# Performance work log

Measured on AMD Instinct MI355X. Metric: run time of the kernel, lower is better.

The kernel has to match this reference:

```python
import jax, jax.numpy as jnp
import numpy as np

EPS = 1e-5  # instance-norm epsilon (NormalizeLayer over spatial axes)

def instance_norm(x):
    # normalize over spatial axes (1,2) per sample, per channel
    mean = jnp.mean(x, axis=(1, 2), keepdims=True)
    var = jnp.var(x, axis=(1, 2), keepdims=True)
    return (x - mean) / jnp.sqrt(var + EPS)

def l2norm(x, axis=-1):
    return x / jnp.sqrt(jnp.sum(x * x, axis=axis, keepdims=True) + 1e-12)

def setup_inputs() -> dict:
    key = jax.random.key(0)
    ks = jax.random.split(key, 5)
    B, H, W, C = 4, 64, 64, 256
    content = jax.random.normal(ks[0], (B, H, W, C), jnp.float32)
    style = jax.random.normal(ks[1], (B, H, W, C), jnp.float32)
    scale = 1.0 / np.sqrt(C)
    Wq = jax.random.normal(ks[2], (C, C), jnp.float32) * scale
    Wk = jax.random.normal(ks[3], (C, C), jnp.float32) * scale
    Wv = jax.random.normal(ks[4], (C, C), jnp.float32) * scale
    bq = jnp.zeros((C,), jnp.float32)
    bk = jnp.zeros((C,), jnp.float32)
    bv = jnp.zeros((C,), jnp.float32)
    return {"content": content, "style": style, "Wq": Wq, "bq": bq,
            "Wk": Wk, "bk": bk, "Wv": Wv, "bv": bv}

def reference(content, style, Wq, bq, Wk, bk, Wv, bv):
    B, H, W, C = content.shape
    N = H * W
    norm_content = instance_norm(content)
    norm_style = instance_norm(style)
    # 1x1 convs == per-pixel linear layers
    Q = (jnp.einsum('bhwc,cd->bhwd', norm_content, Wq) + bq).reshape(B, N, C)
    K = (jnp.einsum('bhwc,cd->bhwd', norm_style, Wk) + bk).reshape(B, N, C)
    V = (jnp.einsum('bhwc,cd->bhwd', style, Wv) + bv).reshape(B, N, C)
    # cosine-similarity attention (Dot with normalize=True)
    attn = jnp.einsum('bnc,bmc->bnm', l2norm(Q), l2norm(K))  # [B, N, N]
    A = jax.nn.softmax(attn, axis=-1)
    M = jnp.einsum('bnm,bmc->bnc', A, V)                 # weighted mean
    S2 = jnp.einsum('bnm,bmc->bnc', A, V * V) - M * M    # weighted variance
    S2 = jax.nn.relu(S2)
    # safe sqrt: grad-safe at exactly 0 (matches sqrt(relu(x)) values)
    S = jnp.where(S2 > 0, jnp.sqrt(jnp.where(S2 > 0, S2, 1.0)), 0.0)
    S = S.reshape(B, H, W, C)
    M = M.reshape(B, H, W, C)
    return S * norm_content + M
```

## Files before the change

### kernel.cpp

```cpp
#include <hip/hip_runtime.h>
#include <cstdint>

#define BB 4
#define NN 4096
#define CC 256

typedef __attribute__((ext_vector_type(8))) short bf16x8;
typedef __attribute__((ext_vector_type(4))) short bf16x4;
typedef __attribute__((ext_vector_type(4))) float f32x4;
typedef unsigned int u32;
typedef __attribute__((ext_vector_type(4))) u32 u32x4;

#define MFMA_FP8(a, b, c)  __builtin_amdgcn_mfma_f32_16x16x32_fp8_fp8((a), (b), (c), 0, 0, 0)

#define WAITCNT(vm, xp, lgkm) (((vm) & 0xF) | (((vm) >> 4) << 14) | ((xp) << 4) | ((lgkm) << 8))

__device__ __forceinline__ unsigned short f2bf(float f) {
  union { float f; unsigned u; } v; v.f = f;
  unsigned r = v.u + 0x7fffu + ((v.u >> 16) & 1u);
  return (unsigned short)(r >> 16);
}
__device__ __forceinline__ u32 pk4_fp8(float a, float b, float c, float d) {
  u32 v = (u32)__builtin_amdgcn_cvt_pk_fp8_f32(a, b, 0, false);
  v = (u32)__builtin_amdgcn_cvt_pk_fp8_f32(c, d, (int)v, true);
  return v;
}
__device__ __forceinline__ unsigned char fp8_1(float a) {
  return (unsigned char)(((u32)__builtin_amdgcn_cvt_pk_fp8_f32(a, a, 0, false)) & 0xff);
}

typedef __attribute__((address_space(3))) unsigned int lds_u32;
typedef __attribute__((address_space(1))) unsigned int glb_u32;

__device__ __forceinline__ void async_cp16(const void* g, void* l) {
  __builtin_amdgcn_global_load_lds((const glb_u32*)g,
                                   (lds_u32*)(unsigned)(unsigned long long)l,
                                   16, 0, 0);
}

__global__ __launch_bounds__(256) void transpose_w(const float* __restrict__ Wq,
                                                   const float* __restrict__ Wk,
                                                   const float* __restrict__ Wv,
                                                   unsigned char* __restrict__ Wt8) {
  __shared__ float sT[64 * 65];
  int blk = blockIdx.x;
  int z = blk / 16, tl = blk % 16;
  int c0 = (tl >> 2) * 64, d0 = (tl & 3) * 64;
  const float* W = (z == 0) ? Wq : ((z == 1) ? Wk : Wv);
  #pragma unroll
  for (int i = 0; i < 16; ++i) {
    int e = i * 256 + threadIdx.x;
    int c = e >> 6, d = e & 63;
    sT[c * 65 + d] = W[(size_t)(c0 + c) * CC + d0 + d];
  }
  __syncthreads();
  #pragma unroll
  for (int i = 0; i < 16; ++i) {
    int e = i * 256 + threadIdx.x;
    int d = e >> 6, c = e & 63;
    Wt8[(size_t)z * 65536 + (size_t)(d0 + d) * CC + c0 + c] = fp8_1(sT[c * 65 + d]);
  }
}

__global__ __launch_bounds__(256) void stats_partial(const float* __restrict__ content,
                                                     const float* __restrict__ style,
                                                     float* __restrict__ sums) {
  int blk = blockIdx.x;
  int t = blk >> 9, b = (blk >> 7) & 3, chunk = blk & 127;
  const float* X = t ? style : content;
  int c = threadIdx.x;
  const float* base = X + ((size_t)b * NN + (size_t)chunk * 32) * CC + c;
  float s = 0.f, ss = 0.f;
  #pragma unroll 8
  for (int r = 0; r < 32; ++r) {
    float x = base[(size_t)r * CC];
    s += x; ss += x * x;
  }
  atomicAdd(&sums[((t * 2 + 0) * BB + b) * CC + c], s);
  atomicAdd(&sums[((t * 2 + 1) * BB + b) * CC + c], ss);
}

__global__ __launch_bounds__(256) void stats_finalize(const float* __restrict__ sums,
                                                      float* __restrict__ stats) {
  int i = blockIdx.x * 256 + threadIdx.x;
  int t = i >> 10, bc = i & 1023;
  float s = sums[(t * 2 + 0) * 1024 + bc];
  float ss = sums[(t * 2 + 1) * 1024 + bc];
  float m = s * (1.0f / NN);
  float var = ss * (1.0f / NN) - m * m;
  stats[(t * 2 + 0) * 1024 + bc] = m;
  stats[(t * 2 + 1) * 1024 + bc] = rsqrtf(var + 1e-5f);
}

__global__ __launch_bounds__(256, 2) void qkv_kernel(
    const float* __restrict__ content, const float* __restrict__ style,
    const unsigned char* __restrict__ Wt8,
    const float* __restrict__ bq, const float* __restrict__ bk, const float* __restrict__ bv,
    const float* __restrict__ stats,
    unsigned char* __restrict__ Qn, unsigned char* __restrict__ Kn,
    unsigned char* __restrict__ Vct) {
  __shared__ __align__(16) char sW[32768];
  __shared__ __align__(16) char sX[32768];

  int tid = threadIdx.x;
  int wid = tid >> 6, lane = tid & 63, quad = lane >> 4, l16 = lane & 15;
  int uwid = __builtin_amdgcn_readfirstlane(wid);
  int tileid = blockIdx.x;
  int z = blockIdx.y;
  int gr0 = tileid * 128;
  int b = gr0 >> 12;

  const float* X = (z == 0) ? content : style;
  int statt = (z == 0) ? 0 : 1;
  const float* mean = stats + ((statt * 2 + 0) * BB + b) * CC;
  const float* rstd = stats + ((statt * 2 + 1) * BB + b) * CC;
  bool donorm = (z < 2);

  #pragma unroll
  for (int i = 0; i < 8; ++i) {
    int lin = i * 256 + tid;
    int row = lin >> 4, c16 = lin & 15;
    int c = c16 * 16;
    const float* xr = X + (size_t)(gr0 + row) * CC + c;
    f32x4 x0 = *(const f32x4*)(xr + 0);
    f32x4 x1 = *(const f32x4*)(xr + 4);
    f32x4 x2 = *(const f32x4*)(xr + 8);
    f32x4 x3 = *(const f32x4*)(xr + 12);
    if (donorm) {
      f32x4 m0 = *(const f32x4*)(mean + c + 0), r0 = *(const f32x4*)(rstd + c + 0);
      f32x4 m1 = *(const f32x4*)(mean + c + 4), r1 = *(const f32x4*)(rstd + c + 4);
      f32x4 m2 = *(const f32x4*)(mean + c + 8), r2 = *(const f32x4*)(rstd + c + 8);
      f32x4 m3 = *(const f32x4*)(mean + c + 12), r3 = *(const f32x4*)(rstd + c + 12);
      x0 = (x0 - m0) * r0; x1 = (x1 - m1) * r1;
      x2 = (x2 - m2) * r2; x3 = (x3 - m3) * r3;
    }
    u32x4 pk;
    pk.x = pk4_fp8(x0.x, x0.y, x0.z, x0.w);
    pk.y = pk4_fp8(x1.x, x1.y, x1.z, x1.w);
    pk.z = pk4_fp8(x2.x, x2.y, x2.z, x2.w);
    pk.w = pk4_fp8(x3.x, x3.y, x3.z, x3.w);
    *(u32x4*)(sX + row * 256 + ((c16 ^ (row & 15)) * 16)) = pk;
  }

  f32x4 zero4 = {0.f, 0.f, 0.f, 0.f};
  f32x4 acc[2][16];
  #pragma unroll
  for (int i = 0; i < 2; ++i)
    #pragma unroll
    for (int j = 0; j < 16; ++j) acc[i][j] = zero4;

  const unsigned char* wb = Wt8 + (size_t)z * 65536;

  for (int half = 0; half < 2; ++half) {
    __syncthreads();
    #pragma unroll
    for (int it = 0; it < 8; ++it) {
      int L = it * 256 + wid * 64 + lane;
      int d = L >> 3;
      int c16 = (L & 7) ^ (d & 7);
      async_cp16(wb + (size_t)d * 256 + half * 128 + c16 * 16,
                 sW + (size_t)(it * 256 + uwid * 64) * 16);
    }
    __syncthreads();

    long a[2][4];
    #pragma unroll
    for (int mf = 0; mf < 2; ++mf) {
      int row = wid * 32 + mf * 16 + l16;
      #pragma unroll
      for (int kc = 0; kc < 4; ++kc) {
        int chunk = half * 8 + kc * 2 + (quad >> 1);
        a[mf][kc] = *(const long*)(sX + row * 256 + ((chunk ^ (row & 15)) * 16) + (quad & 1) * 8);
      }
    }
    #pragma unroll
    for (int nf = 0; nf < 16; ++nf) {
      int d = nf * 16 + l16;
      #pragma unroll
      for (int kc = 0; kc < 4; ++kc) {
        long bw = *(const long*)(sW + d * 128 + (((kc * 2 + (quad >> 1)) ^ (d & 7)) * 16) + (quad & 1) * 8);
        acc[0][nf] = MFMA_FP8(a[0][kc], bw, acc[0][nf]);
        acc[1][nf] = MFMA_FP8(a[1][kc], bw, acc[1][nf]);
      }
    }
  }

  const float* bias = (z == 0) ? bq : ((z == 1) ? bk : bv);
  #pragma unroll
  for (int nf = 0; nf < 16; ++nf) {
    float bb_ = bias[nf * 16 + l16];
    #pragma unroll
    for (int mf = 0; mf < 2; ++mf) {
      acc[mf][nf].x += bb_; acc[mf][nf].y += bb_;
      acc[mf][nf].z += bb_; acc[mf][nf].w += bb_;
    }
  }

  if (z < 2) {
    unsigned char* O = (z == 0) ? Qn : Kn;
    #pragma unroll
    for (int mf = 0; mf < 2; ++mf) {
      f32x4 ss = zero4;
      #pragma unroll
      for (int nf = 0; nf < 16; ++nf) ss += acc[mf][nf] * acc[mf][nf];
      #pragma unroll
      for (int m = 1; m < 16; m <<= 1) {
        ss.x += __shfl_xor(ss.x, m, 64);
        ss.y += __shfl_xor(ss.y, m, 64);
        ss.z += __shfl_xor(ss.z, m, 64);
        ss.w += __shfl_xor(ss.w, m, 64);
      }
      f32x4 rq;
      rq.x = rsqrtf(ss.x + 1e-12f); rq.y = rsqrtf(ss.y + 1e-12f);
      rq.z = rsqrtf(ss.z + 1e-12f); rq.w = rsqrtf(ss.w + 1e-12f);
      int r0 = wid * 32 + mf * 16 + quad * 4;
      #pragma unroll
      for (int nf = 0; nf < 16; ++nf) {
        int col = nf * 16 + l16;
        u32 p01 = (u32)__builtin_amdgcn_cvt_pk_fp8_f32(acc[mf][nf].x * rq.x, acc[mf][nf].y * rq.y, 0, false);
        u32 p23 = (u32)__builtin_amdgcn_cvt_pk_fp8_f32(acc[mf][nf].z * rq.z, acc[mf][nf].w * rq.w, 0, false);
        O[(size_t)(gr0 + r0 + 0) * CC + col] = (unsigned char)(p01 & 0xff);
        O[(size_t)(gr0 + r0 + 1) * CC + col] = (unsigned char)((p01 >> 8) & 0xff);
        O[(size_t)(gr0 + r0 + 2) * CC + col] = (unsigned char)(p23 & 0xff);
        O[(size_t)(gr0 + r0 + 3) * CC + col] = (unsigned char)((p23 >> 8) & 0xff);
      }
    }
  } else {
    char* sOT = sX;
    int n_in_b = gr0 & (NN - 1);
    __syncthreads();
    #pragma unroll
    for (int pass = 0; pass < 2; ++pass) {
      #pragma unroll
      for (int mf = 0; mf < 2; ++mf) {
        int j = wid * 2 + mf;
        int r4 = wid * 32 + mf * 16 + quad * 4;
        (void)r4;
        #pragma unroll
        for (int nf = 0; nf < 16; ++nf) {
          int col = nf * 16 + l16;
          f32x4 v = acc[mf][nf];
          f32x4 w = pass ? (v * v) : v;
          u32 pk = pk4_fp8(w.x, w.y, w.z, w.w);
          *(u32*)(sOT + col * 128 + ((j ^ (col & 7)) * 16) + quad * 4) = pk;
        }
      }
      __syncthreads();
      unsigned char* orow = Vct + ((size_t)(b * 512 + (pass ? 256 : 0) + tid)) * NN + n_in_b;
      #pragma unroll
      for (int j = 0; j < 8; ++j) {
        u32x4 val = *(const u32x4*)(sOT + tid * 128 + ((j ^ (tid & 7)) * 16));
        *(u32x4*)(orow + j * 16) = val;
      }
      __syncthreads();
    }
  }
}

__global__ __launch_bounds__(512, 2) void flash_kernel(
    const unsigned char* __restrict__ Qn,
    const unsigned char* __restrict__ Kn,
    const unsigned char* __restrict__ Vct,
    const float* __restrict__ content,
    const float* __restrict__ stats,
    float* __restrict__ out) {
  __shared__ __align__(16) char smem[32768 + 65536 + 4096 + 256];
  char* sKb = smem;
  char* sVb = smem + 32768;
  char* sP  = smem + 98304;
  float* sL = (float*)(smem + 102400);
  float* sE2 = (float*)smem;

  int tid = threadIdx.x;
  int wid = tid >> 6, lane = tid & 63, quad = lane >> 4, l16 = lane & 15;
  int uwid = __builtin_amdgcn_readfirstlane(wid);

  int id = blockIdx.x;
  int b = (id >> 1) & 3;
  int tile = ((id >> 3) << 1) | (id & 1);
  int q0 = tile * 64;

  int qh = (wid & 1) * 32;
  int kb0 = (wid >> 1) * 16;
  int cw = wid * 64;

  long qf[2][8];
  #pragma unroll
  for (int mf = 0; mf < 2; ++mf) {
    int row = q0 + qh + mf * 16 + l16;
    const unsigned char* base = Qn + (((size_t)b * NN + row) << 8);
    #pragma unroll
    for (int kf = 0; kf < 8; ++kf)
      qf[mf][kf] = *(const long*)(base + kf * 32 + quad * 8);
  }
  __builtin_amdgcn_s_waitcnt(WAITCNT(0, 7, 15));

  if (tid < 64) sL[tid] = 0.f;

  const unsigned char* kbp = Kn + (((size_t)b * NN) << 8);
  const unsigned char* vbp = Vct + ((size_t)b * 512) * NN;

  auto stageK = [&](int k0, int buf) {
    char* dst = sKb + buf * 16384;
    #pragma unroll
    for (int it = 0; it < 2; ++it) {
      int L = it * 512 + wid * 64 + lane;
      int ky = L >> 4, s = L & 15;
      int c16 = s ^ (ky & 15);
      async_cp16(kbp + (((size_t)(k0 + ky)) << 8) + c16 * 16,
                 dst + (size_t)(it * 512 + uwid * 64) * 16);
    }
  };
  auto stageV = [&](int k0, int buf) {
    char* dst = sVb + buf * 32768;
    #pragma unroll
    for (int it = 0; it < 4; ++it) {
      int L = it * 512 + wid * 64 + lane;
      int r128 = L >> 3, s8 = L & 7;
      int x = s8 ^ (r128 & 7);
      int ch = (r128 << 1) | (x >> 2);
      int k16 = x & 3;
      async_cp16(vbp + (size_t)ch * NN + k0 + k16 * 16,
                 dst + (size_t)(it * 512 + uwid * 64) * 16);
    }
  };

  f32x4 zero4 = {0.f, 0.f, 0.f, 0.f};
  f32x4 om[4][4];
  #pragma unroll
  for (int i = 0; i < 4; ++i)
    #pragma unroll
    for (int j = 0; j < 4; ++j) om[i][j] = zero4;
  float Lr[8];
  #pragma unroll
  for (int i = 0; i < 8; ++i) Lr[i] = 0.f;

  stageK(0, 0);  stageV(0, 0);
  stageK(64, 1); stageV(64, 1);

  int keyrow = (kb0 + l16) * 256;
  int key15 = l16;
  int khalf = (quad & 1) * 8;

  for (int kt = 0; kt < 64; ++kt) {
    __builtin_amdgcn_s_waitcnt(WAITCNT(6, 7, 15));
    __builtin_amdgcn_s_barrier();

    const char* sKc = sKb + (kt & 1) * 16384;
    f32x4 s0 = zero4, s1 = zero4;
    #pragma unroll
    for (int kf = 0; kf < 8; ++kf) {
      int slot = (kf * 2 + (quad >> 1)) ^ key15;
      long bk = *(const long*)(sKc + keyrow + slot * 16 + khalf);
      s0 = MFMA_FP8(qf[0][kf], bk, s0);
      s1 = MFMA_FP8(qf[1][kf], bk, s1);
    }
    #pragma unroll
    for (int mf = 0; mf < 2; ++mf) {
      f32x4 sv = mf ? s1 : s0;
      float p0 = __expf(sv.x), p1 = __expf(sv.y), p2 = __expf(sv.z), p3 = __expf(sv.w);
      Lr[mf * 4 + 0] += p0; Lr[mf * 4 + 1] += p1;
      Lr[mf * 4 + 2] += p2; Lr[mf * 4 + 3] += p3;
      u32 b01 = (u32)__builtin_amdgcn_cvt_pk_fp8_f32(p0, p1, 0, false);
      u32 b23 = (u32)__builtin_amdgcn_cvt_pk_fp8_f32(p2, p3, 0, false);
      int qbase = qh + mf * 16 + quad * 4;
      #pragma unroll
      for (int r = 0; r < 4; ++r) {
        int q = qbase + r;
        u32 byte = (r < 2) ? ((r == 0) ? (b01 & 0xff) : ((b01 >> 8) & 0xff))
                           : ((r == 2) ? (b23 & 0xff) : ((b23 >> 8) & 0xff));
        int addr = (q >> 1) * 128 + ((((q & 1) * 4 + (wid >> 1))) ^ ((q >> 1) & 7)) * 16 + l16;
        sP[addr] = (unsigned char)byte;
      }
    }
    __builtin_amdgcn_s_waitcnt(WAITCNT(63, 7, 0));
    __builtin_amdgcn_s_barrier();

    const char* sVc = sVb + (kt & 1) * 32768;
    long pf[2][4], vf[2][4];
    #pragma unroll
    for (int ks = 0; ks < 2; ++ks) {
      int c16 = ks * 2 + (quad >> 1);
      #pragma unroll
      for (int mf2 = 0; mf2 < 4; ++mf2) {
        int q = mf2 * 16 + l16;
        pf[ks][mf2] = *(const long*)(sP + (q >> 1) * 128 +
                        (((q & 1) * 4 + c16) ^ ((q >> 1) & 7)) * 16 + khalf);
      }
      #pragma unroll
      for (int nf = 0; nf < 4; ++nf) {
        int ch = cw + nf * 16 + l16;
        vf[ks][nf] = *(const long*)(sVc + (ch >> 1) * 128 +
                        (((ch & 1) * 4 + c16) ^ ((ch >> 1) & 7)) * 16 + khalf);
      }
    }
    __builtin_amdgcn_s_waitcnt(WAITCNT(63, 7, 0));
    __builtin_amdgcn_s_barrier();

    int nk = ((kt + 2) & 63) * 64;
    stageK(nk, kt & 1);
    stageV(nk, kt & 1);

    #pragma unroll
    for (int ks = 0; ks < 2; ++ks)
      #pragma unroll
      for (int nf = 0; nf < 4; ++nf)
        #pragma unroll
        for (int mf2 = 0; mf2 < 4; ++mf2)
          om[mf2][nf] = MFMA_FP8(pf[ks][mf2], vf[ks][nf], om[mf2][nf]);
  }

  #pragma unroll
  for (int i = 0; i < 8; ++i) {
    #pragma unroll
    for (int m = 1; m < 16; m <<= 1) Lr[i] += __shfl_xor(Lr[i], m, 64);
  }
  if (l16 == 0) {
    #pragma unroll
    for (int mf = 0; mf < 2; ++mf)
      #pragma unroll
      for (int r = 0; r < 4; ++r)
        atomicAdd(&sL[qh + mf * 16 + quad * 4 + r], Lr[mf * 4 + r]);
  }
  __builtin_amdgcn_s_waitcnt(WAITCNT(0, 7, 0));
  __builtin_amdgcn_s_barrier();

  if (wid >= 4) {
    #pragma unroll
    for (int mf2 = 0; mf2 < 4; ++mf2) {
      #pragma unroll
      for (int nf = 0; nf < 4; ++nf) {
        int ch = (wid - 4) * 64 + nf * 16 + l16;
        int cidx = (mf2 * 4 + quad) ^ (ch & 15);
        *(f32x4*)(sE2 + ch * 64 + cidx * 4) = om[mf2][nf];
      }
    }
  }
  __syncthreads();

  if (wid < 4) {
    const float* meanc = stats + (0 * BB + b) * CC;
    const float* rstdc = stats + (1 * BB + b) * CC;
    float linv[4][4];
    #pragma unroll
    for (int mf2 = 0; mf2 < 4; ++mf2)
      #pragma unroll
      for (int r = 0; r < 4; ++r)
        linv[mf2][r] = 1.0f / sL[mf2 * 16 + quad * 4 + r];
    #pragma unroll
    for (int nf = 0; nf < 4; ++nf) {
      int ch = cw + nf * 16 + l16;
      float mc = meanc[ch], rc = rstdc[ch];
      #pragma unroll
      for (int mf2 = 0; mf2 < 4; ++mf2) {
        int cidx = (mf2 * 4 + quad) ^ (ch & 15);
        f32x4 vv = *(const f32x4*)(sE2 + ch * 64 + cidx * 4);
        f32x4 ov = om[mf2][nf];
        #pragma unroll
        for (int r = 0; r < 4; ++r) {
          int row = mf2 * 16 + quad * 4 + r;
          float li = linv[mf2][r];
          float ovr = (r == 0) ? ov.x : (r == 1) ? ov.y : (r == 2) ? ov.z : ov.w;
          float vvr = (r == 0) ? vv.x : (r == 1) ? vv.y : (r == 2) ? vv.z : vv.w;
          float M = ovr * li;
          float E2 = vvr * li;
          float S2 = E2 - M * M;
          float S = (S2 > 0.f) ? sqrtf(S2) : 0.f;
          size_t gi = (((size_t)b * NN + q0 + row) << 8) + ch;
          float xh = (content[gi] - mc) * rc;
          out[gi] = S * xh + M;
        }
      }
    }
  }
}

extern "C" void kernel_launch(void* const* d_in, const int* in_sizes, int n_in,
                              void* d_out, int out_size, void* d_ws, size_t ws_size,
                              hipStream_t stream) {
  const float* content = (const float*)d_in[0];
  const float* style   = (const float*)d_in[1];
  const float* Wq = (const float*)d_in[2];
  const float* bq = (const float*)d_in[3];
  const float* Wk = (const float*)d_in[4];
  const float* bk = (const float*)d_in[5];
  const float* Wv = (const float*)d_in[6];
  const float* bv = (const float*)d_in[7];
  char* ws = (char*)d_ws;

  float* sums        = (float*)(ws + 0);
  float* stats       = (float*)(ws + 16384);
  unsigned char* Wt8 = (unsigned char*)(ws + 32768);
  unsigned char* Qn  = (unsigned char*)(ws + 229376);
  unsigned char* Kn  = (unsigned char*)(ws + 4423680);
  unsigned char* Vct = (unsigned char*)(ws + 8617984);
  float* outp = (float*)d_out;

  hipMemsetAsync(d_ws, 0, 16384, stream);
  hipLaunchKernelGGL(transpose_w, dim3(48), dim3(256), 0, stream, Wq, Wk, Wv, Wt8);
  hipLaunchKernelGGL(stats_partial, dim3(1024), dim3(256), 0, stream, content, style, sums);
  hipLaunchKernelGGL(stats_finalize, dim3(8), dim3(256), 0, stream, sums, stats);
  hipLaunchKernelGGL(qkv_kernel, dim3(128, 3), dim3(256), 0, stream,
                     content, style, Wt8, bq, bk, bv, stats, Qn, Kn, Vct);
  hipLaunchKernelGGL(flash_kernel, dim3(256), dim3(512), 0, stream,
                     Qn, Kn, Vct, content, stats, outp);
}
```

Measured before the change: 233.5 us.

## Software-pipeline score phase with double-buffered P tile and swapped MFMA operands

Restructures the flash attention loop so the QK^T/exp phase for the next key tile runs after the PV MFMAs of the current tile, using a double-buffered P scratch in LDS. This cuts the per-iteration barriers from three to one. It also swaps the MFMA operand order so each lane holds four keys for one query, which allows packed 32-bit P writes instead of byte stores and simplifies the row-sum reduction. The cost is extra LDS and more live registers, which could lower occupancy.

```diff
diff --git a/kernel.cpp b/kernel.cpp
--- a/kernel.cpp
+++ b/kernel.cpp
@@ -234,8 +234,6 @@
       #pragma unroll
       for (int mf = 0; mf < 2; ++mf) {
         int j = wid * 2 + mf;
-        int r4 = wid * 32 + mf * 16 + quad * 4;
-        (void)r4;
         #pragma unroll
         for (int nf = 0; nf < 16; ++nf) {
           int col = nf * 16 + l16;
@@ -264,11 +262,11 @@
     const float* __restrict__ content,
     const float* __restrict__ stats,
     float* __restrict__ out) {
-  __shared__ __align__(16) char smem[32768 + 65536 + 4096 + 256];
+  __shared__ __align__(16) char smem[32768 + 65536 + 8192 + 256];
   char* sKb = smem;
   char* sVb = smem + 32768;
-  char* sP  = smem + 98304;
-  float* sL = (float*)(smem + 102400);
+  char* sPb = smem + 98304;
+  float* sL = (float*)(smem + 106496);
   float* sE2 = (float*)smem;
 
   int tid = threadIdx.x;
@@ -286,12 +284,12 @@
 
   long qf[2][8];
   #pragma unroll
-  for (int mf = 0; mf < 2; ++mf) {
-    int row = q0 + qh + mf * 16 + l16;
+  for (int ng = 0; ng < 2; ++ng) {
+    int row = q0 + qh + ng * 16 + l16;
     const unsigned char* base = Qn + (((size_t)b * NN + row) << 8);
     #pragma unroll
     for (int kf = 0; kf < 8; ++kf)
-      qf[mf][kf] = *(const long*)(base + kf * 32 + quad * 8);
+      qf[ng][kf] = *(const long*)(base + kf * 32 + quad * 8);
   }
   __builtin_amdgcn_s_waitcnt(WAITCNT(0, 7, 15));
 
@@ -331,62 +329,38 @@
   for (int i = 0; i < 4; ++i)
     #pragma unroll
     for (int j = 0; j < 4; ++j) om[i][j] = zero4;
-  float Lr[8];
-  #pragma unroll
-  for (int i = 0; i < 8; ++i) Lr[i] = 0.f;
-
-  stageK(0, 0);  stageV(0, 0);
-  stageK(64, 1); stageV(64, 1);
-
-  int keyrow = (kb0 + l16) * 256;
-  int key15 = l16;
+  float Lr[2] = {0.f, 0.f};
+  long vf[2][4];
+
+  int krow = kb0 + l16;
+  int krowoff = krow * 256;
   int khalf = (quad & 1) * 8;
 
-  for (int kt = 0; kt < 64; ++kt) {
-    __builtin_amdgcn_s_waitcnt(WAITCNT(6, 7, 15));
-    __builtin_amdgcn_s_barrier();
-
+  auto s_phase = [&](int kt) {
     const char* sKc = sKb + (kt & 1) * 16384;
-    f32x4 s0 = zero4, s1 = zero4;
+    char* sPc = sPb + (kt & 1) * 4096;
+    f32x4 t0 = zero4, t1 = zero4;
     #pragma unroll
     for (int kf = 0; kf < 8; ++kf) {
-      int slot = (kf * 2 + (quad >> 1)) ^ key15;
-      long bk = *(const long*)(sKc + keyrow + slot * 16 + khalf);
-      s0 = MFMA_FP8(qf[0][kf], bk, s0);
-      s1 = MFMA_FP8(qf[1][kf], bk, s1);
-    }
-    #pragma unroll
-    for (int mf = 0; mf < 2; ++mf) {
-      f32x4 sv = mf ? s1 : s0;
+      int slot = (kf * 2 + (quad >> 1)) ^ (krow & 15);
+      long ak = *(const long*)(sKc + krowoff + slot * 16 + khalf);
+      t0 = MFMA_FP8(ak, qf[0][kf], t0);
+      t1 = MFMA_FP8(ak, qf[1][kf], t1);
+    }
+    #pragma unroll
+    for (int ng = 0; ng < 2; ++ng) {
+      f32x4 sv = ng ? t1 : t0;
       float p0 = __expf(sv.x), p1 = __expf(sv.y), p2 = __expf(sv.z), p3 = __expf(sv.w);
-      Lr[mf * 4 + 0] += p0; Lr[mf * 4 + 1] += p1;
-      Lr[mf * 4 + 2] += p2; Lr[mf * 4 + 3] += p3;
-      u32 b01 = (u32)__builtin_amdgcn_cvt_pk_fp8_f32(p0, p1, 0, false);
-      u32 b23 = (u32)__builtin_amdgcn_cvt_pk_fp8_f32(p2, p3, 0, false);
-      int qbase = qh + mf * 16 + quad * 4;
-      #pragma unroll
-      for (int r = 0; r < 4; ++r) {
-        int q = qbase + r;
-        u32 byte = (r < 2) ? ((r == 0) ? (b01 & 0xff) : ((b01 >> 8) & 0xff))
-                           : ((r == 2) ? (b23 & 0xff) : ((b23 >> 8) & 0xff));
-        int addr = (q >> 1) * 128 + ((((q & 1) * 4 + (wid >> 1))) ^ ((q >> 1) & 7)) * 16 + l16;
-        sP[addr] = (unsigned char)byte;
-      }
-    }
-    __builtin_amdgcn_s_waitcnt(WAITCNT(63, 7, 0));
-    __builtin_amdgcn_s_barrier();
-
+      Lr[ng] += p0 + p1 + p2 + p3;
+      u32 w = pk4_fp8(p0, p1, p2, p3);
+      int q = qh + ng * 16 + l16;
+      int c = (kb0 >> 2) + quad;
+      *(u32*)(sPc + q * 64 + ((c ^ (q & 14)) * 4)) = w;
+    }
     const char* sVc = sVb + (kt & 1) * 32768;
-    long pf[2][4], vf[2][4];
     #pragma unroll
     for (int ks = 0; ks < 2; ++ks) {
       int c16 = ks * 2 + (quad >> 1);
-      #pragma unroll
-      for (int mf2 = 0; mf2 < 4; ++mf2) {
-        int q = mf2 * 16 + l16;
-        pf[ks][mf2] = *(const long*)(sP + (q >> 1) * 128 +
-                        (((q & 1) * 4 + c16) ^ ((q >> 1) & 7)) * 16 + khalf);
-      }
       #pragma unroll
       for (int nf = 0; nf < 4; ++nf) {
         int ch = cw + nf * 16 + l16;
@@ -394,45 +368,67 @@
                         (((ch & 1) * 4 + c16) ^ ((ch >> 1) & 7)) * 16 + khalf);
       }
     }
-    __builtin_amdgcn_s_waitcnt(WAITCNT(63, 7, 0));
-    __builtin_amdgcn_s_barrier();
-
+  };
+
+  stageK(0, 0);  stageV(0, 0);
+  stageK(64, 1); stageV(64, 1);
+  __builtin_amdgcn_s_waitcnt(WAITCNT(6, 7, 15));
+  __builtin_amdgcn_s_barrier();
+  s_phase(0);
+  __builtin_amdgcn_s_waitcnt(WAITCNT(63, 7, 0));
+  __builtin_amdgcn_s_barrier();
+
+  for (int kt = 0; kt < 64; ++kt) {
     int nk = ((kt + 2) & 63) * 64;
     stageK(nk, kt & 1);
     stageV(nk, kt & 1);
 
+    const char* sPc = sPb + (kt & 1) * 4096;
+    long pf[2][4];
+    #pragma unroll
+    for (int ks = 0; ks < 2; ++ks)
+      #pragma unroll
+      for (int mf = 0; mf < 4; ++mf) {
+        int q = mf * 16 + l16;
+        int c = ks * 8 + quad * 2;
+        pf[ks][mf] = *(const long*)(sPc + q * 64 + ((c ^ (q & 14)) * 4));
+      }
+
     #pragma unroll
     for (int ks = 0; ks < 2; ++ks)
       #pragma unroll
       for (int nf = 0; nf < 4; ++nf)
         #pragma unroll
-        for (int mf2 = 0; mf2 < 4; ++mf2)
-          om[mf2][nf] = MFMA_FP8(pf[ks][mf2], vf[ks][nf], om[mf2][nf]);
-  }
-
-  #pragma unroll
-  for (int i = 0; i < 8; ++i) {
-    #pragma unroll
-    for (int m = 1; m < 16; m <<= 1) Lr[i] += __shfl_xor(Lr[i], m, 64);
-  }
-  if (l16 == 0) {
-    #pragma unroll
-    for (int mf = 0; mf < 2; ++mf)
-      #pragma unroll
-      for (int r = 0; r < 4; ++r)
-        atomicAdd(&sL[qh + mf * 16 + quad * 4 + r], Lr[mf * 4 + r]);
+        for (int mf = 0; mf < 4; ++mf)
+          om[mf][nf] = MFMA_FP8(pf[ks][mf], vf[ks][nf], om[mf][nf]);
+
+    __builtin_amdgcn_s_waitcnt(WAITCNT(6, 7, 15));
+    if (kt < 63) s_phase(kt + 1);
+
+    __builtin_amdgcn_s_waitcnt(WAITCNT(63, 7, 0));
+    __builtin_amdgcn_s_barrier();
+  }
+
+  #pragma unroll
+  for (int ng = 0; ng < 2; ++ng) {
+    Lr[ng] += __shfl_xor(Lr[ng], 16, 64);
+    Lr[ng] += __shfl_xor(Lr[ng], 32, 64);
+  }
+  if (quad == 0) {
+    atomicAdd(&sL[qh + 0 + l16], Lr[0]);
+    atomicAdd(&sL[qh + 16 + l16], Lr[1]);
   }
   __builtin_amdgcn_s_waitcnt(WAITCNT(0, 7, 0));
   __builtin_amdgcn_s_barrier();
 
   if (wid >= 4) {
     #pragma unroll
-    for (int mf2 = 0; mf2 < 4; ++mf2) {
+    for (int mf = 0; mf < 4; ++mf) {
       #pragma unroll
       for (int nf = 0; nf < 4; ++nf) {
         int ch = (wid - 4) * 64 + nf * 16 + l16;
-        int cidx = (mf2 * 4 + quad) ^ (ch & 15);
-        *(f32x4*)(sE2 + ch * 64 + cidx * 4) = om[mf2][nf];
+        int cidx = (mf * 4 + quad) ^ (ch & 15);
+        *(f32x4*)(sE2 + ch * 64 + cidx * 4) = om[mf][nf];
       }
     }
   }
@@ -443,23 +439,23 @@
     const float* rstdc = stats + (1 * BB + b) * CC;
     float linv[4][4];
     #pragma unroll
-    for (int mf2 = 0; mf2 < 4; ++mf2)
+    for (int mf = 0; mf < 4; ++mf)
       #pragma unroll
       for (int r = 0; r < 4; ++r)
-        linv[mf2][r] = 1.0f / sL[mf2 * 16 + quad * 4 + r];
+        linv[mf][r] = 1.0f / sL[mf * 16 + quad * 4 + r];
     #pragma unroll
     for (int nf = 0; nf < 4; ++nf) {
       int ch = cw + nf * 16 + l16;
       float mc = meanc[ch], rc = rstdc[ch];
       #pragma unroll
-      for (int mf2 = 0; mf2 < 4; ++mf2) {
-        int cidx = (mf2 * 4 + quad) ^ (ch & 15);
+      for (int mf = 0; mf < 4; ++mf) {
+        int cidx = (mf * 4 + quad) ^ (ch & 15);
         f32x4 vv = *(const f32x4*)(sE2 + ch * 64 + cidx * 4);
-        f32x4 ov = om[mf2][nf];
+        f32x4 ov = om[mf][nf];
         #pragma unroll
         for (int r = 0; r < 4; ++r) {
-          int row = mf2 * 16 + quad * 4 + r;
-          float li = linv[mf2][r];
+          int row = mf * 16 + quad * 4 + r;
+          float li = linv[mf][r];
           float ovr = (r == 0) ? ov.x : (r == 1) ? ov.y : (r == 2) ? ov.z : ov.w;
           float vvr = (r == 0) ? vv.x : (r == 1) ? vv.y : (r == 2) ? vv.z : vv.w;
           float M = ovr * li;
```

New measurement: 207.4 us. 1.13x faster.
